# Kernel optimization log

Measured on AMD Instinct MI355X. Metric: run time of the kernel, lower is better.

The kernel has to match this reference:

```python
import jax, jax.numpy as jnp
import numpy as np

# Regularized layout for the per-batch masked attention:
#   batch_size B=8, each batch has NF=2048 'fill' points followed by NK=4096 'keep' points.
B, NF, NK = 8, 2048, 4096
C_IN, C_KQ, C_OUT = 256, 64, 256


def setup_inputs() -> dict:
    key = jax.random.key(0)
    ks = jax.random.split(key, 7)
    N = B * (NF + NK)
    features = jax.random.normal(ks[0], (N, C_IN), dtype=jnp.float32)
    # keep flag: 0 for fill points, 1 for keep points, per batch (fill-first layout)
    flag = jnp.tile(jnp.concatenate([jnp.zeros(NF, jnp.int32), jnp.ones(NK, jnp.int32)]), B)
    s = 1.0 / np.sqrt(C_IN)
    Wq = jax.random.normal(ks[1], (C_KQ, C_IN), jnp.float32) * s
    bq = jnp.zeros((C_KQ,), jnp.float32)
    Wk = jax.random.normal(ks[2], (C_KQ, C_IN), jnp.float32) * s
    bk = jnp.zeros((C_KQ,), jnp.float32)
    Wv = jax.random.normal(ks[3], (C_OUT, C_IN), jnp.float32) * s
    bv = jnp.zeros((C_OUT,), jnp.float32)
    return {"features": features, "keep_flag": flag,
            "Wq": Wq, "bq": bq, "Wk": Wk, "bk": bk, "Wv": Wv, "bv": bv}


def reference(features, keep_flag, Wq, bq, Wk, bk, Wv, bv):
    # features: [N, C_IN]; keep_flag encodes the fill/keep split, which in this
    # regular layout is: first NF rows of each batch are fill, remaining NK are keep.
    del keep_flag  # structure is encoded in the layout (fill-first per batch)
    f = features.reshape(B, NF + NK, C_IN)
    fill = f[:, :NF]             # [B, NF, C_IN]
    keep = f[:, NF:]             # [B, NK, C_IN]
    q = fill @ Wq.T + bq         # [B, NF, C_KQ]
    k = keep @ Wk.T + bk         # [B, NK, C_KQ]
    v = keep @ Wv.T + bv         # [B, NK, C_OUT]
    ratio = np.sqrt(C_KQ).astype(np.float32)
    scores = jnp.einsum('bfd,bkd->bfk', q, k) / ratio   # [B, NF, NK]
    attn = jax.nn.softmax(scores, axis=-1)
    out_fill = jnp.einsum('bfk,bkc->bfc', attn, v)      # [B, NF, C_OUT]
    # keep rows pass through unchanged (only fill rows are overwritten)
    out = jnp.concatenate([out_fill, keep], axis=1)
    return out.reshape(B * (NF + NK), C_OUT)
```

## Files before the change

### kernel.cpp

```cpp
#include <hip/hip_runtime.h>
#include <hip/hip_bf16.h>

#define BATCHES 8
#define NFILL 2048
#define NKEEP 4096
#define SEQLEN 6144
#define CIN 256
#define CKQ 64
#define COUT 256

#define KSC 0.18033688011112042f
#define KOFF -11.541560327111707f

typedef __bf16 bf16_t;
typedef float f32x4 __attribute__((ext_vector_type(4)));
typedef bf16_t bf16x8 __attribute__((ext_vector_type(8)));
typedef bf16_t bf16x4 __attribute__((ext_vector_type(4)));

__device__ inline void cvt8_store(bf16_t* dst, float4 a, float4 b) {
  bf16x8 v;
  v[0] = (bf16_t)a.x; v[1] = (bf16_t)a.y; v[2] = (bf16_t)a.z; v[3] = (bf16_t)a.w;
  v[4] = (bf16_t)b.x; v[5] = (bf16_t)b.y; v[6] = (bf16_t)b.z; v[7] = (bf16_t)b.w;
  *(bf16x8*)dst = v;
}

__global__ __launch_bounds__(256, 3) void gemm_qkv(
    const float* __restrict__ feat, const float* __restrict__ Wq,
    const float* __restrict__ bq, const float* __restrict__ Wk,
    const float* __restrict__ bk, const float* __restrict__ Wv,
    const float* __restrict__ bv, bf16_t* __restrict__ Qw,
    bf16_t* __restrict__ Kw, bf16_t* __restrict__ Vw,
    float* __restrict__ outp) {
  __shared__ bf16_t Xs[64][264];
  __shared__ bf16_t Ws[2][64][72];

  const int bid = blockIdx.x;
  const bool isQ = bid >= 512;
  const int mb = isQ ? bid - 512 : bid;

  const int t = threadIdx.x;
  const int lane = t & 63;
  const int wv = t >> 6;
  const int l16 = lane & 15;
  const int quad = lane >> 4;

  const int lr = t >> 2;
  const int koff = (t & 3) << 4;

  const int mrow = mb * 64 + lr;
  const int rpb_shift = isQ ? 11 : 12;
  const int batch = mrow >> rpb_shift;
  const int ridx = mrow & ((1 << rpb_shift) - 1);
  const int row_off = isQ ? 0 : NFILL;
  const long grow = (long)(batch * SEQLEN + row_off + ridx);
  const float* xptr = feat + grow * CIN;
  float4* orow = (float4*)(outp + grow * COUT);

  const int NT = isQ ? 1 : 5;
  const int G = NT * 4;
  const float* w0src = isQ ? Wq : Wk;

#define WCHUNK_PTR(g)                                                        \
  (((g) < 4 ? w0src : Wv + (long)((((g) >> 2) - 1) * 64) * CIN) +            \
   (long)lr * CIN + ((g)&3) * 64 + koff)

  float4 wr[2][4];
  {
    const float* wp = WCHUNK_PTR(0);
#pragma unroll
    for (int s = 0; s < 4; s++) wr[0][s] = *(const float4*)(wp + s * 4);
  }

#pragma unroll
  for (int j = 0; j < 4; j++) {
    const int c = koff + j * 64;
    float4 x0 = *(const float4*)(xptr + c);
    float4 x1 = *(const float4*)(xptr + c + 4);
    float4 x2 = *(const float4*)(xptr + c + 8);
    float4 x3 = *(const float4*)(xptr + c + 12);
    cvt8_store(&Xs[lr][c], x0, x1);
    cvt8_store(&Xs[lr][c + 8], x2, x3);
    if (!isQ) {
      orow[(c >> 2) + 0] = x0;
      orow[(c >> 2) + 1] = x1;
      orow[(c >> 2) + 2] = x2;
      orow[(c >> 2) + 3] = x3;
    }
  }
  cvt8_store(&Ws[0][lr][koff], wr[0][0], wr[0][1]);
  cvt8_store(&Ws[0][lr][koff + 8], wr[0][2], wr[0][3]);
  {
    const float* wp = WCHUNK_PTR(1);
#pragma unroll
    for (int s = 0; s < 4; s++) wr[1][s] = *(const float4*)(wp + s * 4);
  }
  asm volatile("s_waitcnt lgkmcnt(0)\n\ts_barrier" ::: "memory");

  const int vb = (mb * 64) >> 12;
  const int key0base = (mb * 64) & 4095;

  f32x4 acc[4];
#pragma unroll 1
  for (int nt = 0; nt < NT; nt++) {
#pragma unroll
    for (int nb = 0; nb < 4; nb++) acc[nb] = f32x4{0.f, 0.f, 0.f, 0.f};

#pragma unroll
    for (int kc = 0; kc < 4; kc++) {
      const int g = nt * 4 + kc;
      const int cb = g & 1;
      const bool last = (g + 1 == G);

      if (!last) {
        cvt8_store(&Ws[cb ^ 1][lr][koff], wr[cb ^ 1][0], wr[cb ^ 1][1]);
        cvt8_store(&Ws[cb ^ 1][lr][koff + 8], wr[cb ^ 1][2], wr[cb ^ 1][3]);
      }
      if (g + 2 < G) {
        const float* wp = WCHUNK_PTR(g + 2);
#pragma unroll
        for (int s = 0; s < 4; s++) wr[cb][s] = *(const float4*)(wp + s * 4);
      }

      if (nt == 0) {
#pragma unroll
        for (int ks = 0; ks < 2; ks++) {
          bf16x8 afrag =
              *(const bf16x8*)&Xs[wv * 16 + l16][kc * 64 + ks * 32 + quad * 8];
#pragma unroll
          for (int nb = 0; nb < 4; nb++) {
            bf16x8 bfrag = *(const bf16x8*)&Ws[cb][nb * 16 + l16][ks * 32 + quad * 8];
            acc[nb] = __builtin_amdgcn_mfma_f32_16x16x32_bf16(afrag, bfrag, acc[nb], 0, 0, 0);
          }
        }
      } else {
#pragma unroll
        for (int ks = 0; ks < 2; ks++) {
          bf16x8 xfrag =
              *(const bf16x8*)&Xs[wv * 16 + l16][kc * 64 + ks * 32 + quad * 8];
#pragma unroll
          for (int nb = 0; nb < 4; nb++) {
            bf16x8 wfrag = *(const bf16x8*)&Ws[cb][nb * 16 + l16][ks * 32 + quad * 8];
            acc[nb] = __builtin_amdgcn_mfma_f32_16x16x32_bf16(wfrag, xfrag, acc[nb], 0, 0, 0);
          }
        }
      }

      if (!last)
        asm volatile("s_waitcnt lgkmcnt(0)\n\ts_barrier" ::: "memory");
    }

    if (nt == 0) {
      const float* bias = isQ ? bq : bk;
      bf16_t* op = isQ ? Qw : Kw;
#pragma unroll
      for (int nb = 0; nb < 4; nb++) {
        const int n = nb * 16 + l16;
        const float bb = bias[n];
#pragma unroll
        for (int r = 0; r < 4; r++) {
          const int m = mb * 64 + wv * 16 + quad * 4 + r;
          op[(long)m * CKQ + n] = (bf16_t)(acc[nb][r] + bb);
        }
      }
    } else {
      const int n0 = (nt - 1) * 64;
#pragma unroll
      for (int nb = 0; nb < 4; nb++) {
        f32x4 bbv = *(const f32x4*)&bv[n0 + nb * 16 + quad * 4];
        bf16_t* vdst = Vw +
                       ((long)(vb * COUT + n0 + nb * 16 + quad * 4)) * NKEEP +
                       key0base + wv * 16 + l16;
#pragma unroll
        for (int r = 0; r < 4; r++)
          vdst[(long)r * NKEEP] = (bf16_t)(acc[nb][r] + bbv[r]);
      }
    }
  }
#undef WCHUNK_PTR
}

__global__ __launch_bounds__(256) void attn_kernel(
    const bf16_t* __restrict__ Q, const bf16_t* __restrict__ K,
    const bf16_t* __restrict__ Vt, float* __restrict__ outp) {
  __shared__ bf16_t Ks[2][64][72];
  __shared__ bf16_t Ps[64][72];
  __shared__ float Lsh[64];

  const int b = blockIdx.x & 7;
  const int qt = blockIdx.x >> 3;
  const int t = threadIdx.x;
  const int lane = t & 63;
  const int wv = t >> 6;
  const int l16 = lane & 15;
  const int quad = lane >> 4;

  const int krow = t >> 2;
  const int kcol = (t & 3) << 4;

  const bf16_t* kbase = K + (long)b * NKEEP * CKQ;
  const int c0 = wv * 64;
  const bf16_t* vlane =
      Vt + ((long)(b * COUT + c0 + l16)) * NKEEP + quad * 8;

  bf16x8 qfrag[2];
  {
    const bf16_t* qrow = Q + ((long)(b * NFILL + qt * 64 + wv * 16 + l16)) * CKQ;
#pragma unroll
    for (int ks = 0; ks < 2; ks++)
      qfrag[ks] = *(const bf16x8*)(qrow + ks * 32 + quad * 8);
  }

  f32x4 oacc[4][4];
#pragma unroll
  for (int m = 0; m < 4; m++)
#pragma unroll
    for (int ct = 0; ct < 4; ct++) oacc[m][ct] = f32x4{0.f, 0.f, 0.f, 0.f};
  float rsum = 0.f;

  uint4 kreg0, kreg1;
  bf16x8 vA[8], vB[8];

  {
    const bf16_t* ksrc = kbase + (long)krow * CKQ + kcol;
    uint4 k0 = *(const uint4*)ksrc;
    uint4 k1 = *(const uint4*)(ksrc + 8);
#pragma unroll
    for (int ct = 0; ct < 4; ct++)
#pragma unroll
      for (int ks = 0; ks < 2; ks++)
        vA[ct * 2 + ks] = *(const bf16x8*)(vlane + (long)ct * 16 * NKEEP + ks * 32);
    *(uint4*)&Ks[0][krow][kcol] = k0;
    *(uint4*)&Ks[0][krow][kcol + 8] = k1;
  }

#define ATTN_TILE(BUF, VCUR, VNEXT, TV)                                         \
  {                                                                             \
    __syncthreads(); \
    const int tn = ((TV) + 1 < 64) ? (TV) + 1 : 63;                             \
    {                                                                           \
      const bf16_t* ksrc = kbase + ((long)(tn * 64 + krow)) * CKQ + kcol;       \
      kreg0 = *(const uint4*)ksrc;                                              \
      kreg1 = *(const uint4*)(ksrc + 8);                                        \
      const bf16_t* vsrc = vlane + (long)tn * 64;                               \
      _Pragma("unroll") for (int ct = 0; ct < 4; ct++)                          \
          _Pragma("unroll") for (int ks = 0; ks < 2; ks++)                      \
              VNEXT[ct * 2 + ks] =                                              \
          *(const bf16x8*)(vsrc + (long)ct * 16 * NKEEP + ks * 32);             \
    }                                                                           \
    f32x4 sacc[4];   \
    _Pragma("unroll") for (int kb = 0; kb < 4; kb++)                            \
        sacc[kb] = f32x4{0.f, 0.f, 0.f, 0.f};                                   \
    _Pragma("unroll") for (int ks = 0; ks < 2; ks++) {                          \
      _Pragma("unroll") for (int kb = 0; kb < 4; kb++) {                        \
        bf16x8 kfrag = *(const bf16x8*)&Ks[BUF][kb * 16 + l16][ks * 32 + quad * 8]; \
        sacc[kb] = __builtin_amdgcn_mfma_f32_16x16x32_bf16(kfrag, qfrag[ks],    \
                                                           sacc[kb], 0, 0, 0); \
      }                                                                         \
    }                                                                           \
    _Pragma("unroll") for (int kb = 0; kb < 4; kb++) {                          \
      const float e0 = __builtin_exp2f(fmaf(sacc[kb][0], KSC, KOFF));           \
      const float e1 = __builtin_exp2f(fmaf(sacc[kb][1], KSC, KOFF));           \
      const float e2 = __builtin_exp2f(fmaf(sacc[kb][2], KSC, KOFF));           \
      const float e3 = __builtin_exp2f(fmaf(sacc[kb][3], KSC, KOFF));           \
      rsum += (e0 + e1) + (e2 + e3);                                            \
      bf16x4 pk;                                                                \
      pk[0] = (bf16_t)e0; pk[1] = (bf16_t)e1;                                   \
      pk[2] = (bf16_t)e2; pk[3] = (bf16_t)e3;                                   \
      *(bf16x4*)&Ps[wv * 16 + l16][kb * 16 + quad * 4] = pk;                    \
    }                                                                           \
    asm volatile("s_waitcnt lgkmcnt(0)\n\ts_barrier" ::: "memory");      \
    _Pragma("unroll") for (int ks = 0; ks < 2; ks++) {                          \
      _Pragma("unroll") for (int m = 0; m < 4; m++) {                           \
        bf16x8 pfrag = *(const bf16x8*)&Ps[m * 16 + l16][ks * 32 + quad * 8];   \
        _Pragma("unroll") for (int ct = 0; ct < 4; ct++)                        \
            oacc[m][ct] = __builtin_amdgcn_mfma_f32_16x16x32_bf16(              \
                pfrag, VCUR[ct * 2 + ks], oacc[m][ct], 0, 0, 0);                \
      }                                                                         \
    }                                                                           \
    *(uint4*)&Ks[BUF ^ 1][krow][kcol] = kreg0;                                  \
    *(uint4*)&Ks[BUF ^ 1][krow][kcol + 8] = kreg1;                              \
  }

#pragma unroll 1
  for (int tv = 0; tv < 64; tv += 2) {
    ATTN_TILE(0, vA, vB, tv)
    ATTN_TILE(1, vB, vA, tv + 1)
  }
#undef ATTN_TILE

  rsum += __shfl_xor(rsum, 16, 64);
  rsum += __shfl_xor(rsum, 32, 64);
  if (quad == 0) Lsh[wv * 16 + l16] = rsum;
  __syncthreads();

  float rl[4][4];
#pragma unroll
  for (int m = 0; m < 4; m++)
#pragma unroll
    for (int r = 0; r < 4; r++) rl[m][r] = 1.0f / Lsh[m * 16 + quad * 4 + r];

  const long obase = ((long)(b * SEQLEN + qt * 64)) * COUT + c0;
#pragma unroll
  for (int m = 0; m < 4; m++)
#pragma unroll
    for (int ct = 0; ct < 4; ct++)
#pragma unroll
      for (int r = 0; r < 4; r++)
        outp[obase + (long)(m * 16 + quad * 4 + r) * COUT + ct * 16 + l16] =
            oacc[m][ct][r] * rl[m][r];
}

extern "C" void kernel_launch(void* const* d_in, const int* in_sizes, int n_in,
                              void* d_out, int out_size, void* d_ws, size_t ws_size,
                              hipStream_t stream) {
  const float* feat = (const float*)d_in[0];
  const float* Wq = (const float*)d_in[2];
  const float* bq = (const float*)d_in[3];
  const float* Wk = (const float*)d_in[4];
  const float* bk = (const float*)d_in[5];
  const float* Wv = (const float*)d_in[6];
  const float* bv = (const float*)d_in[7];
  float* outp = (float*)d_out;

  bf16_t* Qw = (bf16_t*)d_ws;
  bf16_t* Kw = Qw + (size_t)BATCHES * NFILL * CKQ;
  bf16_t* Vw = Kw + (size_t)BATCHES * NKEEP * CKQ;

  gemm_qkv<<<dim3(768), 256, 0, stream>>>(feat, Wq, bq, Wk, bk, Wv, bv,
                                          Qw, Kw, Vw, outp);
  attn_kernel<<<dim3(NFILL / 64 * BATCHES), 256, 0, stream>>>(Qw, Kw, Vw, outp);
}
```

Before: 207.8 us.

## Split attention over two key halves and combine partial sums in a second kernel

Attention is split along the key dimension into two halves, doubling the grid from 256 to 512 blocks so more of the GPU's compute units are busy. Each block writes unnormalized partial outputs (half 0 into the output buffer, half 1 into workspace) plus row sums, and a combine kernel adds them and normalizes. This relies on the fixed exponent offset (no running max), so partial sums combine directly. The cost is extra fp32 traffic for the partial outputs and one more kernel launch; the original kernel remains as a fallback when the workspace is too small.

```diff
diff --git a/kernel.cpp b/kernel.cpp
--- a/kernel.cpp
+++ b/kernel.cpp
@@ -179,15 +179,18 @@
 #undef WCHUNK_PTR
 }
 
-__global__ __launch_bounds__(256) void attn_kernel(
+__global__ __launch_bounds__(256) void attn_split(
     const bf16_t* __restrict__ Q, const bf16_t* __restrict__ K,
-    const bf16_t* __restrict__ Vt, float* __restrict__ outp) {
+    const bf16_t* __restrict__ Vt, float* __restrict__ outp,
+    float* __restrict__ O1, float* __restrict__ Lbuf) {
   __shared__ bf16_t Ks[2][64][72];
   __shared__ bf16_t Ps[64][72];
-  __shared__ float Lsh[64];
 
   const int b = blockIdx.x & 7;
-  const int qt = blockIdx.x >> 3;
+  const int idx = blockIdx.x >> 3;
+  const int qt = idx & 31;
+  const int kh = idx >> 5;
+  const int t0 = kh * 32;
   const int t = threadIdx.x;
   const int lane = t & 63;
   const int wv = t >> 6;
@@ -221,14 +224,15 @@
   bf16x8 vA[8], vB[8];
 
   {
-    const bf16_t* ksrc = kbase + (long)krow * CKQ + kcol;
+    const bf16_t* ksrc = kbase + ((long)(t0 * 64 + krow)) * CKQ + kcol;
     uint4 k0 = *(const uint4*)ksrc;
     uint4 k1 = *(const uint4*)(ksrc + 8);
+    const bf16_t* vsrc = vlane + (long)t0 * 64;
 #pragma unroll
     for (int ct = 0; ct < 4; ct++)
 #pragma unroll
       for (int ks = 0; ks < 2; ks++)
-        vA[ct * 2 + ks] = *(const bf16x8*)(vlane + (long)ct * 16 * NKEEP + ks * 32);
+        vA[ct * 2 + ks] = *(const bf16x8*)(vsrc + (long)ct * 16 * NKEEP + ks * 32);
     *(uint4*)&Ks[0][krow][kcol] = k0;
     *(uint4*)&Ks[0][krow][kcol + 8] = k1;
   }
@@ -282,6 +286,159 @@
   }
 
 #pragma unroll 1
+  for (int tv = t0; tv < t0 + 32; tv += 2) {
+    ATTN_TILE(0, vA, vB, tv)
+    ATTN_TILE(1, vB, vA, tv + 1)
+  }
+#undef ATTN_TILE
+
+  rsum += __shfl_xor(rsum, 16, 64);
+  rsum += __shfl_xor(rsum, 32, 64);
+  if (quad == 0)
+    Lbuf[(((kh * 8) + b) * 32 + qt) * 64 + wv * 16 + l16] = rsum;
+
+  float* obuf = kh ? (O1 + ((long)((b * 32 + qt) * 64)) * COUT)
+                   : (outp + ((long)(b * SEQLEN + qt * 64)) * COUT);
+#pragma unroll
+  for (int m = 0; m < 4; m++)
+#pragma unroll
+    for (int ct = 0; ct < 4; ct++)
+#pragma unroll
+      for (int r = 0; r < 4; r++)
+        obuf[(long)(m * 16 + quad * 4 + r) * COUT + c0 + ct * 16 + l16] =
+            oacc[m][ct][r];
+}
+
+__global__ __launch_bounds__(256) void attn_combine(
+    const float* __restrict__ O1, const float* __restrict__ Lbuf,
+    float* __restrict__ outp) {
+  const int b = blockIdx.x & 7;
+  const int qt = blockIdx.x >> 3;
+  const int t = threadIdx.x;
+  const int row = t >> 2;
+  const int cseg = (t & 3) * 64;
+
+  const float L0 = Lbuf[((0 * 8 + b) * 32 + qt) * 64 + row];
+  const float L1 = Lbuf[((1 * 8 + b) * 32 + qt) * 64 + row];
+  const float rl = 1.0f / (L0 + L1);
+
+  float4* dst = (float4*)(outp + ((long)(b * SEQLEN + qt * 64) + row) * COUT + cseg);
+  const float4* s1 = (const float4*)(O1 + ((long)((b * 32 + qt) * 64) + row) * COUT + cseg);
+#pragma unroll
+  for (int j = 0; j < 16; j++) {
+    float4 a = dst[j];
+    float4 c = s1[j];
+    a.x = (a.x + c.x) * rl;
+    a.y = (a.y + c.y) * rl;
+    a.z = (a.z + c.z) * rl;
+    a.w = (a.w + c.w) * rl;
+    dst[j] = a;
+  }
+}
+
+__global__ __launch_bounds__(256) void attn_kernel(
+    const bf16_t* __restrict__ Q, const bf16_t* __restrict__ K,
+    const bf16_t* __restrict__ Vt, float* __restrict__ outp) {
+  __shared__ bf16_t Ks[2][64][72];
+  __shared__ bf16_t Ps[64][72];
+  __shared__ float Lsh[64];
+
+  const int b = blockIdx.x & 7;
+  const int qt = blockIdx.x >> 3;
+  const int t = threadIdx.x;
+  const int lane = t & 63;
+  const int wv = t >> 6;
+  const int l16 = lane & 15;
+  const int quad = lane >> 4;
+
+  const int krow = t >> 2;
+  const int kcol = (t & 3) << 4;
+
+  const bf16_t* kbase = K + (long)b * NKEEP * CKQ;
+  const int c0 = wv * 64;
+  const bf16_t* vlane =
+      Vt + ((long)(b * COUT + c0 + l16)) * NKEEP + quad * 8;
+
+  bf16x8 qfrag[2];
+  {
+    const bf16_t* qrow = Q + ((long)(b * NFILL + qt * 64 + wv * 16 + l16)) * CKQ;
+#pragma unroll
+    for (int ks = 0; ks < 2; ks++)
+      qfrag[ks] = *(const bf16x8*)(qrow + ks * 32 + quad * 8);
+  }
+
+  f32x4 oacc[4][4];
+#pragma unroll
+  for (int m = 0; m < 4; m++)
+#pragma unroll
+    for (int ct = 0; ct < 4; ct++) oacc[m][ct] = f32x4{0.f, 0.f, 0.f, 0.f};
+  float rsum = 0.f;
+
+  uint4 kreg0, kreg1;
+  bf16x8 vA[8], vB[8];
+
+  {
+    const bf16_t* ksrc = kbase + (long)krow * CKQ + kcol;
+    uint4 k0 = *(const uint4*)ksrc;
+    uint4 k1 = *(const uint4*)(ksrc + 8);
+#pragma unroll
+    for (int ct = 0; ct < 4; ct++)
+#pragma unroll
+      for (int ks = 0; ks < 2; ks++)
+        vA[ct * 2 + ks] = *(const bf16x8*)(vlane + (long)ct * 16 * NKEEP + ks * 32);
+    *(uint4*)&Ks[0][krow][kcol] = k0;
+    *(uint4*)&Ks[0][krow][kcol + 8] = k1;
+  }
+
+#define ATTN_TILE(BUF, VCUR, VNEXT, TV)                                         \
+  {                                                                             \
+    __syncthreads();                                                            \
+    const int tn = ((TV) + 1 < 64) ? (TV) + 1 : 63;                             \
+    {                                                                           \
+      const bf16_t* ksrc = kbase + ((long)(tn * 64 + krow)) * CKQ + kcol;       \
+      kreg0 = *(const uint4*)ksrc;                                              \
+      kreg1 = *(const uint4*)(ksrc + 8);                                        \
+      const bf16_t* vsrc = vlane + (long)tn * 64;                               \
+      _Pragma("unroll") for (int ct = 0; ct < 4; ct++)                          \
+          _Pragma("unroll") for (int ks = 0; ks < 2; ks++)                      \
+              VNEXT[ct * 2 + ks] =                                              \
+          *(const bf16x8*)(vsrc + (long)ct * 16 * NKEEP + ks * 32);             \
+    }                                                                           \
+    f32x4 sacc[4];                                                              \
+    _Pragma("unroll") for (int kb = 0; kb < 4; kb++)                            \
+        sacc[kb] = f32x4{0.f, 0.f, 0.f, 0.f};                                   \
+    _Pragma("unroll") for (int ks = 0; ks < 2; ks++) {                          \
+      _Pragma("unroll") for (int kb = 0; kb < 4; kb++) {                        \
+        bf16x8 kfrag = *(const bf16x8*)&Ks[BUF][kb * 16 + l16][ks * 32 + quad * 8]; \
+        sacc[kb] = __builtin_amdgcn_mfma_f32_16x16x32_bf16(kfrag, qfrag[ks],    \
+                                                           sacc[kb], 0, 0, 0); \
+      }                                                                         \
+    }                                                                           \
+    _Pragma("unroll") for (int kb = 0; kb < 4; kb++) {                          \
+      const float e0 = __builtin_exp2f(fmaf(sacc[kb][0], KSC, KOFF));           \
+      const float e1 = __builtin_exp2f(fmaf(sacc[kb][1], KSC, KOFF));           \
+      const float e2 = __builtin_exp2f(fmaf(sacc[kb][2], KSC, KOFF));           \
+      const float e3 = __builtin_exp2f(fmaf(sacc[kb][3], KSC, KOFF));           \
+      rsum += (e0 + e1) + (e2 + e3);                                            \
+      bf16x4 pk;                                                                \
+      pk[0] = (bf16_t)e0; pk[1] = (bf16_t)e1;                                   \
+      pk[2] = (bf16_t)e2; pk[3] = (bf16_t)e3;                                   \
+      *(bf16x4*)&Ps[wv * 16 + l16][kb * 16 + quad * 4] = pk;                    \
+    }                                                                           \
+    asm volatile("s_waitcnt lgkmcnt(0)\n\ts_barrier" ::: "memory");             \
+    _Pragma("unroll") for (int ks = 0; ks < 2; ks++) {                          \
+      _Pragma("unroll") for (int m = 0; m < 4; m++) {                           \
+        bf16x8 pfrag = *(const bf16x8*)&Ps[m * 16 + l16][ks * 32 + quad * 8];   \
+        _Pragma("unroll") for (int ct = 0; ct < 4; ct++)                        \
+            oacc[m][ct] = __builtin_amdgcn_mfma_f32_16x16x32_bf16(              \
+                pfrag, VCUR[ct * 2 + ks], oacc[m][ct], 0, 0, 0);                \
+      }                                                                         \
+    }                                                                           \
+    *(uint4*)&Ks[BUF ^ 1][krow][kcol] = kreg0;                                  \
+    *(uint4*)&Ks[BUF ^ 1][krow][kcol + 8] = kreg1;                              \
+  }
+
+#pragma unroll 1
   for (int tv = 0; tv < 64; tv += 2) {
     ATTN_TILE(0, vA, vB, tv)
     ATTN_TILE(1, vB, vA, tv + 1)
@@ -325,8 +482,20 @@
   bf16_t* Qw = (bf16_t*)d_ws;
   bf16_t* Kw = Qw + (size_t)BATCHES * NFILL * CKQ;
   bf16_t* Vw = Kw + (size_t)BATCHES * NKEEP * CKQ;
+  float* O1 = (float*)(Vw + (size_t)BATCHES * COUT * NKEEP);
+  float* Lb = O1 + (size_t)BATCHES * 32 * 64 * COUT;
+
+  const size_t need =
+      ((size_t)BATCHES * NFILL * CKQ + (size_t)BATCHES * NKEEP * CKQ +
+       (size_t)BATCHES * COUT * NKEEP) * sizeof(bf16_t) +
+      ((size_t)BATCHES * 32 * 64 * COUT + 2u * BATCHES * 32 * 64) * sizeof(float);
 
   gemm_qkv<<<dim3(768), 256, 0, stream>>>(feat, Wq, bq, Wk, bk, Wv, bv,
                                           Qw, Kw, Vw, outp);
-  attn_kernel<<<dim3(NFILL / 64 * BATCHES), 256, 0, stream>>>(Qw, Kw, Vw, outp);
+  if (ws_size >= need) {
+    attn_split<<<dim3(512), 256, 0, stream>>>(Qw, Kw, Vw, outp, O1, Lb);
+    attn_combine<<<dim3(256), 256, 0, stream>>>(O1, Lb, outp);
+  } else {
+    attn_kernel<<<dim3(256), 256, 0, stream>>>(Qw, Kw, Vw, outp);
+  }
 }
```

Measured after the change: 214.8 us. +3.4%, slower.
